# Kernel optimization log

Hardware: AMD Instinct MI355X
Metric: run time of the kernel (lower is better)

The kernel has to match this reference:

```python
import jax, jax.numpy as jnp
import numpy as np

EPS = 1e-8


def setup_inputs() -> dict:
    key = jax.random.key(0)
    k1, k2, k3, k4 = jax.random.split(key, 4)
    batch, n_obs, hist = 64, 2048, 512
    values = jax.random.normal(k1, (batch, n_obs, hist), dtype=jnp.float32)
    means = jax.random.normal(k2, (n_obs,), dtype=jnp.float32)
    counts = jax.random.randint(k3, (n_obs,), 0, 1000, dtype=jnp.int32)
    # M2 = var * count, keep it positive and roughly scaled with count
    M2s = jax.random.uniform(k4, (n_obs,), dtype=jnp.float32) * counts.astype(jnp.float32)
    sig_ids = jnp.arange(n_obs, dtype=jnp.int32)  # one unique signature per obs column
    return {"values": values, "means": means, "M2s": M2s, "counts": counts, "sig_ids": sig_ids}


def reference(values, means, M2s, counts, sig_ids):
    """Training-mode forward: Welford merge of running per-signature stats with the
    batch of last-timestep values, then normalize full history with merged stats.

    values: [b, n, h] float; means/M2s: [n_sigs]; counts: [n_sigs] int; sig_ids: [n] int.
    """
    b = values.shape[0]
    v = values[:, :, -1]                      # [b, n] last timestep per obs
    mean_new = jnp.mean(v, axis=0)            # [n]
    var_new = jnp.var(v, axis=0)              # biased (ddof=0), matches unbiased=False
    count_new = jnp.float32(b)
    M2_new = var_new * count_new              # [n]

    # gather prior stats per observation column
    c = counts[sig_ids].astype(jnp.float32)   # [n]
    m = means[sig_ids]                        # [n]
    M2 = M2s[sig_ids]                         # [n]

    # Welford parallel merge (matches update())
    delta = mean_new - m
    total = c + count_new
    m_merged = m + delta * (count_new / total)
    M2_merged = M2 + M2_new + delta * delta * c * count_new / total

    # stats are stored detached (torch.no_grad + .detach())
    m_merged = jax.lax.stop_gradient(m_merged)
    M2_merged = jax.lax.stop_gradient(M2_merged)
    total = jax.lax.stop_gradient(total)

    var = M2_merged / total
    std = jnp.sqrt(var + EPS)                 # [n]
    normed = (values - m_merged[None, :, None]) / std[None, :, None]
    # count < 2 -> passthrough (matches normalize())
    ok = (total >= 2.0)[None, :, None]
    return jnp.where(ok, normed, values)
```

## Files before the change

kernel.cpp:

```cpp
#include <hip/hip_runtime.h>
#include <math.h>

#define EPS 1e-8f

__global__ void sig_stats_kernel(const float* __restrict__ values,
                                 const float* __restrict__ means,
                                 const float* __restrict__ M2s,
                                 const int* __restrict__ counts,
                                 const int* __restrict__ sig_ids,
                                 float* __restrict__ scale,
                                 float* __restrict__ shift,
                                 int n_obs, int hist, int batch) {
    int wave = (int)((blockIdx.x * blockDim.x + threadIdx.x) >> 6);
    int lane = (int)(threadIdx.x & 63);
    if (wave >= n_obs) return;

    float v = 0.0f;
    if (lane < batch) {
        long long idx = (long long)lane * n_obs * hist + (long long)wave * hist + (hist - 1);
        v = values[idx];
    }

    float s = v;
    #pragma unroll
    for (int o = 32; o > 0; o >>= 1) s += __shfl_xor(s, o, 64);
    float cnt_new = (float)batch;
    float mean_new = s / cnt_new;

    float d = (lane < batch) ? (v - mean_new) : 0.0f;
    float sq = d * d;
    #pragma unroll
    for (int o = 32; o > 0; o >>= 1) sq += __shfl_xor(sq, o, 64);
    float M2_new = sq;

    if (lane == 0) {
        int id = sig_ids[wave];
        float c  = (float)counts[id];
        float m  = means[id];
        float M2 = M2s[id];
        float delta = mean_new - m;
        float total = c + cnt_new;
        float m_merged  = m + delta * (cnt_new / total);
        float M2_merged = M2 + M2_new + delta * delta * c * cnt_new / total;
        float var = M2_merged / total;
        float stdv = sqrtf(var + EPS);
        bool ok = (total >= 2.0f);
        float sc = ok ? (1.0f / stdv) : 1.0f;
        float sh = ok ? (-m_merged / stdv) : 0.0f;
        scale[wave] = sc;
        shift[wave] = sh;
    }
}

__global__ void sig_norm_kernel(const float4* __restrict__ vals,
                                const float* __restrict__ scale,
                                const float* __restrict__ shift,
                                float4* __restrict__ out,
                                int n_obs, int h4) {
    int row = blockIdx.x;
    int n = row % n_obs;
    float s = scale[n];
    float t = shift[n];
    long long base = (long long)row * h4;
    for (int j = threadIdx.x; j < h4; j += blockDim.x) {
        float4 v = vals[base + j];
        float4 o;
        o.x = fmaf(v.x, s, t);
        o.y = fmaf(v.y, s, t);
        o.z = fmaf(v.z, s, t);
        o.w = fmaf(v.w, s, t);
        out[base + j] = o;
    }
}

extern "C" void kernel_launch(void* const* d_in, const int* in_sizes, int n_in,
                              void* d_out, int out_size, void* d_ws, size_t ws_size,
                              hipStream_t stream) {
    const float* values  = (const float*)d_in[0];
    const float* means   = (const float*)d_in[1];
    const float* M2s     = (const float*)d_in[2];
    const int*   counts  = (const int*)d_in[3];
    const int*   sig_ids = (const int*)d_in[4];
    float* out = (float*)d_out;

    const int batch = 64;
    int n_obs = in_sizes[1];
    long long total = (long long)in_sizes[0];
    int hist = (int)(total / ((long long)batch * n_obs));

    float* scale = (float*)d_ws;
    float* shift = scale + n_obs;

    int waves_per_block = 4;
    int blocks1 = (n_obs + waves_per_block - 1) / waves_per_block;
    sig_stats_kernel<<<blocks1, 256, 0, stream>>>(values, means, M2s, counts, sig_ids,
                                                  scale, shift, n_obs, hist, batch);

    int h4 = hist / 4;
    int rows = batch * n_obs;
    sig_norm_kernel<<<rows, 128, 0, stream>>>((const float4*)values, scale, shift,
                                              (float4*)out, n_obs, h4);
}
```

Baseline: 428.5 us.

## Fuse stats and normalization into one kernel with one block per observation

```diff
diff --git a/kernel.cpp b/kernel.cpp
--- a/kernel.cpp
+++ b/kernel.cpp
@@ -3,73 +3,74 @@
 
 #define EPS 1e-8f
 
-__global__ void sig_stats_kernel(const float* __restrict__ values,
-                                 const float* __restrict__ means,
-                                 const float* __restrict__ M2s,
-                                 const int* __restrict__ counts,
-                                 const int* __restrict__ sig_ids,
-                                 float* __restrict__ scale,
-                                 float* __restrict__ shift,
-                                 int n_obs, int hist, int batch) {
-    int wave = (int)((blockIdx.x * blockDim.x + threadIdx.x) >> 6);
-    int lane = (int)(threadIdx.x & 63);
-    if (wave >= n_obs) return;
+__global__ __launch_bounds__(256) void sig_fused_kernel(
+    const float* __restrict__ values,
+    const float* __restrict__ means,
+    const float* __restrict__ M2s,
+    const int* __restrict__ counts,
+    const int* __restrict__ sig_ids,
+    float* __restrict__ out,
+    int n_obs, int hist, int batch) {
+    const int n    = blockIdx.x;
+    const int tid  = (int)threadIdx.x;
+    const int lane = tid & 63;
+    const int wave = tid >> 6;
 
-    float v = 0.0f;
-    if (lane < batch) {
-        long long idx = (long long)lane * n_obs * hist + (long long)wave * hist + (hist - 1);
-        v = values[idx];
+    __shared__ float s_sc, s_sh;
+
+    if (wave == 0) {
+        float v = 0.0f;
+        if (lane < batch) {
+            long long idx = ((long long)lane * n_obs + n) * hist + (hist - 1);
+            v = values[idx];
+        }
+        float s = v;
+        #pragma unroll
+        for (int o = 32; o > 0; o >>= 1) s += __shfl_xor(s, o, 64);
+        const float cnt_new  = (float)batch;
+        const float mean_new = s / cnt_new;
+        float d  = (lane < batch) ? (v - mean_new) : 0.0f;
+        float sq = d * d;
+        #pragma unroll
+        for (int o = 32; o > 0; o >>= 1) sq += __shfl_xor(sq, o, 64);
+
+        if (lane == 0) {
+            const int   id = sig_ids[n];
+            const float c  = (float)counts[id];
+            const float m  = means[id];
+            const float M2 = M2s[id];
+            const float delta     = mean_new - m;
+            const float total     = c + cnt_new;
+            const float m_merged  = m + delta * (cnt_new / total);
+            const float M2_merged = M2 + sq + delta * delta * c * cnt_new / total;
+            const float var  = M2_merged / total;
+            const float stdv = sqrtf(var + EPS);
+            const bool  ok   = (total >= 2.0f);
+            s_sc = ok ? (1.0f / stdv)      : 1.0f;
+            s_sh = ok ? (-m_merged / stdv) : 0.0f;
+        }
     }
+    __syncthreads();
 
-    float s = v;
-    #pragma unroll
-    for (int o = 32; o > 0; o >>= 1) s += __shfl_xor(s, o, 64);
-    float cnt_new = (float)batch;
-    float mean_new = s / cnt_new;
+    const float sc = s_sc;
+    const float sh = s_sh;
 
-    float d = (lane < batch) ? (v - mean_new) : 0.0f;
-    float sq = d * d;
-    #pragma unroll
-    for (int o = 32; o > 0; o >>= 1) sq += __shfl_xor(sq, o, 64);
-    float M2_new = sq;
+    const int h4 = hist >> 2;
+    const float4* __restrict__ vin  = (const float4*)values;
+    float4*       __restrict__ vout = (float4*)out;
+    const int nwaves = (int)blockDim.x >> 6;
 
-    if (lane == 0) {
-        int id = sig_ids[wave];
-        float c  = (float)counts[id];
-        float m  = means[id];
-        float M2 = M2s[id];
-        float delta = mean_new - m;
-        float total = c + cnt_new;
-        float m_merged  = m + delta * (cnt_new / total);
-        float M2_merged = M2 + M2_new + delta * delta * c * cnt_new / total;
-        float var = M2_merged / total;
-        float stdv = sqrtf(var + EPS);
-        bool ok = (total >= 2.0f);
-        float sc = ok ? (1.0f / stdv) : 1.0f;
-        float sh = ok ? (-m_merged / stdv) : 0.0f;
-        scale[wave] = sc;
-        shift[wave] = sh;
-    }
-}
-
-__global__ void sig_norm_kernel(const float4* __restrict__ vals,
-                                const float* __restrict__ scale,
-                                const float* __restrict__ shift,
-                                float4* __restrict__ out,
-                                int n_obs, int h4) {
-    int row = blockIdx.x;
-    int n = row % n_obs;
-    float s = scale[n];
-    float t = shift[n];
-    long long base = (long long)row * h4;
-    for (int j = threadIdx.x; j < h4; j += blockDim.x) {
-        float4 v = vals[base + j];
-        float4 o;
-        o.x = fmaf(v.x, s, t);
-        o.y = fmaf(v.y, s, t);
-        o.z = fmaf(v.z, s, t);
-        o.w = fmaf(v.w, s, t);
-        out[base + j] = o;
+    for (int b = wave; b < batch; b += nwaves) {
+        const long long base = ((long long)b * n_obs + n) * h4;
+        for (int j = lane; j < h4; j += 64) {
+            float4 v = vin[base + j];
+            float4 o;
+            o.x = fmaf(v.x, sc, sh);
+            o.y = fmaf(v.y, sc, sh);
+            o.z = fmaf(v.z, sc, sh);
+            o.w = fmaf(v.w, sc, sh);
+            vout[base + j] = o;
+        }
     }
 }
 
@@ -88,16 +89,6 @@
     long long total = (long long)in_sizes[0];
     int hist = (int)(total / ((long long)batch * n_obs));
 
-    float* scale = (float*)d_ws;
-    float* shift = scale + n_obs;
-
-    int waves_per_block = 4;
-    int blocks1 = (n_obs + waves_per_block - 1) / waves_per_block;
-    sig_stats_kernel<<<blocks1, 256, 0, stream>>>(values, means, M2s, counts, sig_ids,
-                                                  scale, shift, n_obs, hist, batch);
-
-    int h4 = hist / 4;
-    int rows = batch * n_obs;
-    sig_norm_kernel<<<rows, 128, 0, stream>>>((const float4*)values, scale, shift,
-                                              (float4*)out, n_obs, h4);
+    sig_fused_kernel<<<n_obs, 256, 0, stream>>>(values, means, M2s, counts, sig_ids,
+                                                out, n_obs, hist, batch);
 }
```

Result: slower. 460.6 us (+7.5%).
